# Performance work log

Measured on AMD Instinct MI355X. Metric: run time of the kernel, lower is better.

The kernel has to match this reference:

```python
import jax, jax.numpy as jnp
import numpy as np
import math

B, N, D, K = 8, 2048, 1024, 128
PI = math.pi


def setup_inputs() -> dict:
    key = jax.random.key(0)
    ks = jax.random.split(key, 4)
    x = jax.random.normal(ks[0], (B, N, D), dtype=jnp.float32)
    W_proj = jax.random.normal(ks[1], (D, 6 * K), dtype=jnp.float32) * (D ** -0.5)
    # structured bias init as in OscillatorProjection._init_weights
    b = np.zeros(6 * K, np.float32)
    groups = [K // 4, K // 2, K - K // 4 - K // 2]
    centers = [0.3, 0.65, 0.97]
    off = 3 * K
    for n_k, c in zip(groups, centers):
        b[off:off + n_k] = math.log(c / (1.0 - c))
        off += n_k
    b[4 * K:5 * K] = math.log(0.65 / 0.35)
    b[5 * K:] = -2.0
    b_proj = jnp.asarray(b)
    omega_base = jnp.exp(jnp.linspace(math.log(2.0 * PI / N), math.log(PI * (1.0 - 1.0 / K)), K)).astype(jnp.float32)
    W_phase = jax.random.normal(ks[2], (D, K), dtype=jnp.float32) * 0.001
    b_phase = jnp.zeros((K,), jnp.float32)
    W_res = jax.random.normal(ks[3], (4 * K - 2, D), dtype=jnp.float32) * 0.002
    lambda_pcg = jnp.float32(0.5)
    res_scale = jnp.float32(0.05)
    return dict(x=x, W_proj=W_proj, b_proj=b_proj, omega_base=omega_base,
                W_phase=W_phase, b_phase=b_phase, W_res=W_res,
                lambda_pcg=lambda_pcg, res_scale=res_scale)


def _resonance_scan(alpha, drive):
    # linear recurrence r_t = alpha_t * r_{t-1} + d_t, r_0 = 0, along axis=1
    def combine(e1, e2):
        a1, b1 = e1
        a2, b2 = e2
        return (a2 * a1, a2 * b1 + b2)
    _, r = jax.lax.associative_scan(combine, (alpha, drive), axis=1)
    return r


def reference(x, W_proj, b_proj, omega_base, W_phase, b_phase, W_res, lambda_pcg, res_scale):
    _, n, _ = x.shape
    out = x @ W_proj + b_proj  # [B, n, 6K]
    A_r, Om_r, Ph_r, Ga_r, Go_r, Be_r = jnp.split(out, 6, axis=-1)
    A = jnp.minimum(jax.nn.softplus(A_r), 3.0)
    omega = jnp.clip(jax.nn.sigmoid(Om_r) * PI + omega_base, 1e-4, PI - 1e-4)
    phi = jnp.tanh(Ph_r) * PI
    alpha = jax.nn.sigmoid(Ga_r)
    g_out = jax.nn.sigmoid(Go_r)
    beta = jax.nn.sigmoid(Be_r)
    positions = jnp.log1p(jnp.arange(n, dtype=jnp.float32)).reshape(1, n, 1)
    angle = omega * positions + phi
    cos_a = jnp.cos(angle)
    sin_a = jnp.sin(angle)
    drive = (1.0 - alpha) * A
    # fused real/imag scan sharing alpha (mirrors the fused Triton path)
    r = _resonance_scan(jnp.concatenate([alpha, alpha], axis=-1),
                        jnp.concatenate([drive * cos_a, drive * sin_a], axis=-1))
    r_r, r_i = r[..., :K], r[..., K:]
    readout = r_r * cos_a + r_i * sin_a
    r_r = r_r - beta * readout * cos_a
    r_i = r_i - beta * readout * sin_a
    # state norm: rescale only when |r| > 1
    modulus = jnp.sqrt(r_r ** 2 + r_i ** 2 + 1e-8)
    scale = jnp.maximum(modulus, 1.0)
    r_r = r_r / scale
    r_i = r_i / scale
    # rotate into the oscillator frame
    rho_re = r_r * cos_a + r_i * sin_a
    rho_im = -r_r * sin_a + r_i * cos_a
    rho_norm = jnp.sqrt(rho_re ** 2 + rho_im ** 2 + 1e-6)
    pq = x @ W_phase + b_phase
    align = (rho_re * jnp.cos(pq) + rho_im * jnp.sin(pq)) / rho_norm
    gate = jax.nn.sigmoid(lambda_pcg * align)
    rho_re = gate * rho_re
    rho_im = gate * rho_im
    # SCPM: adjacent-oscillator complex cross products -> 4K-2 features
    cross_re = rho_re[..., :-1] * rho_re[..., 1:] + rho_im[..., :-1] * rho_im[..., 1:]
    cross_im = rho_im[..., :-1] * rho_re[..., 1:] - rho_re[..., :-1] * rho_im[..., 1:]
    feats = jnp.concatenate([g_out * rho_re, g_out * rho_im, cross_re, cross_im], axis=-1)
    return x + res_scale * (feats @ W_res)
```

## Files before the change

kernel.cpp:

```cpp
#include <hip/hip_runtime.h>
#include <math.h>

#define PI_F 3.14159265358979323846f
#define SEG 128
#define SLEN 16
typedef unsigned short u16;
typedef __attribute__((ext_vector_type(8))) short bf16x8;
typedef __attribute__((ext_vector_type(4))) float f32x4;

__device__ __forceinline__ float sigmoidf_(float x){ return __fdividef(1.0f, 1.0f+__expf(-x)); }
__device__ __forceinline__ float softplusf_(float x){
    return fmaxf(x, 0.f) + __logf(1.f + __expf(-fabsf(x)));
}
__device__ __forceinline__ float tanhpi_(float x){
    float t = __expf(-2.f*fabsf(x));
    float th = __fdividef(1.f - t, 1.f + t);
    return copysignf(th, x)*PI_F;
}
__device__ __forceinline__ void fsincos(float a, float* s, float* c){
    float r = a * 0.15915494309189535f;
    r = r - floorf(r);
#if __has_builtin(__builtin_amdgcn_sinf)
    *s = __builtin_amdgcn_sinf(r);
    *c = __builtin_amdgcn_cosf(r);
#else
    float t = r * 6.283185307179586f;
    *s = __sinf(t); *c = __cosf(t);
#endif
}
__device__ __forceinline__ u16 f2bf(float f){
    unsigned u = __float_as_uint(f);
    return (u16)((u + 0x7FFFu + ((u>>16)&1u)) >> 16);
}
__device__ __forceinline__ float b2f(u16 v){
    return __uint_as_float(((unsigned)v)<<16);
}
__device__ __forceinline__ void gl_lds16(const u16* g, u16* l){
    __builtin_amdgcn_global_load_lds((const __attribute__((address_space(1))) void*)g,
                                     (__attribute__((address_space(3))) void*)l, 16, 0, 0);
}

__global__ __launch_bounds__(256) void k_cvt_x(const float* __restrict__ x, u16* __restrict__ xb){
    size_t i = ((size_t)blockIdx.x*256 + threadIdx.x)*8;
    float4 v0 = *(const float4*)&x[i];
    float4 v1 = *(const float4*)&x[i+4];
    ushort4 a = make_ushort4(f2bf(v0.x),f2bf(v0.y),f2bf(v0.z),f2bf(v0.w));
    ushort4 b = make_ushort4(f2bf(v1.x),f2bf(v1.y),f2bf(v1.z),f2bf(v1.w));
    *(ushort4*)&xb[i]   = a;
    *(ushort4*)&xb[i+4] = b;
}

__global__ __launch_bounds__(256) void k_tcvt(const float* __restrict__ W, u16* __restrict__ Wt,
                                              int K, int Ns, int KD){
    __shared__ float s[32][33];
    const int tx = threadIdx.x & 31, ty = threadIdx.x >> 5;
    const int k0 = blockIdx.y*32, n0 = blockIdx.x*32;
    #pragma unroll
    for (int i=0;i<4;i++){
        int k = k0 + ty + i*8;
        s[ty+i*8][tx] = (k < K) ? W[(size_t)k*Ns + n0 + tx] : 0.f;
    }
    __syncthreads();
    #pragma unroll
    for (int i=0;i<4;i++){
        int n = n0 + ty + i*8;
        Wt[(size_t)n*KD + k0 + tx] = f2bf(s[tx][ty+i*8]);
    }
}

__global__ __launch_bounds__(512,1) void k_mm1(
    const u16* __restrict__ A,
    const u16* __restrict__ Bt,
    const float* __restrict__ bp, const float* __restrict__ bph,
    u16* __restrict__ C)
{
    __shared__ u16 sm[3*16384];
    const int bid = blockIdx.x;
    const int swz = (bid & 7)*32 + (bid >> 3);
    const int by = swz >> 2, bx = swz & 3;
    const int r0 = by*256, c0 = bx*256;
    const int tid = threadIdx.x;
    const int w = tid >> 6, lane = tid & 63;
    const int wm = w >> 2, wn = w & 3;
    const int lr = lane & 15, lk = lane >> 4;

    const u16* gA = A  + (size_t)(r0 + w*32 + (lane>>2))*1024 + (lane&3)*8;
    const u16* gB = Bt + (size_t)(c0 + w*32 + (lane>>2))*1024 + (lane&3)*8;
    const int ldsA = w*1024;
    const int ldsB = 8192 + w*1024;

    const int aoff = (wm*128 + lr)*32 + lk*8;
    const int boff = 8192 + (wn*64 + lr)*32 + lk*8;

    f32x4 acc[8][4] = {};

    #pragma unroll
    for (int j=0;j<2;j++){
        gl_lds16(gA + j*16*1024,      sm + ldsA + j*512);
        gl_lds16(gB + j*16*1024,      sm + ldsB + j*512);
    }
    #pragma unroll
    for (int j=0;j<2;j++){
        gl_lds16(gA + j*16*1024 + 32, sm + 16384 + ldsA + j*512);
        gl_lds16(gB + j*16*1024 + 32, sm + 16384 + ldsB + j*512);
    }
    asm volatile("s_waitcnt vmcnt(4)" ::: "memory");
    __builtin_amdgcn_s_barrier();
    __builtin_amdgcn_sched_barrier(0);

    for (int k=0; k<32; ++k){
        const u16* bufp = sm + (k%3)*16384;
        u16*       bufn = sm + ((k+2)%3)*16384;
        const int  k0n  = (k+2)*32;
        bf16x8 af[4], bfr[4];

        #pragma unroll
        for (int m=0;m<4;m++) af[m]  = *(const bf16x8*)&bufp[aoff + m*512];
        #pragma unroll
        for (int n=0;n<4;n++) bfr[n] = *(const bf16x8*)&bufp[boff + n*512];
        if (k < 30){
            gl_lds16(gA + k0n,           bufn + ldsA);
            gl_lds16(gA + 16*1024 + k0n, bufn + ldsA + 512);
        }
        __builtin_amdgcn_s_barrier();
        __builtin_amdgcn_sched_barrier(0);
        asm volatile("s_waitcnt lgkmcnt(0)" ::: "memory");
        __builtin_amdgcn_sched_barrier(0);
        __builtin_amdgcn_s_setprio(1);
        #pragma unroll
        for (int m=0;m<4;m++)
            #pragma unroll
            for (int n=0;n<4;n++)
                acc[m][n] = __builtin_amdgcn_mfma_f32_16x16x32_bf16(af[m], bfr[n], acc[m][n],0,0,0);
        __builtin_amdgcn_s_setprio(0);
        __builtin_amdgcn_s_barrier();
        __builtin_amdgcn_sched_barrier(0);

        #pragma unroll
        for (int m=0;m<4;m++) af[m] = *(const bf16x8*)&bufp[aoff + (m+4)*512];
        if (k < 30){
            gl_lds16(gB + k0n,           bufn + ldsB);
            gl_lds16(gB + 16*1024 + k0n, bufn + ldsB + 512);
        }
        __builtin_amdgcn_s_barrier();
        __builtin_amdgcn_sched_barrier(0);
        asm volatile("s_waitcnt lgkmcnt(0)" ::: "memory");
        __builtin_amdgcn_sched_barrier(0);
        __builtin_amdgcn_s_setprio(1);
        #pragma unroll
        for (int m=0;m<4;m++)
            #pragma unroll
            for (int n=0;n<4;n++)
                acc[m+4][n] = __builtin_amdgcn_mfma_f32_16x16x32_bf16(af[m], bfr[n], acc[m+4][n],0,0,0);
        __builtin_amdgcn_s_setprio(0);
        if (k < 30)       asm volatile("s_waitcnt vmcnt(4)" ::: "memory");
        else if (k == 30) asm volatile("s_waitcnt vmcnt(0)" ::: "memory");
        __builtin_amdgcn_s_barrier();
        __builtin_amdgcn_sched_barrier(0);
    }

    if (c0 + wn*64 < 896){
        #pragma unroll
        for (int n=0;n<4;n++){
            const int col = c0 + wn*64 + n*16 + lr;
            const float bl = (col < 768) ? bp[col] : bph[col-768];
            #pragma unroll
            for (int m=0;m<8;m++){
                const int row = r0 + wm*128 + m*16 + lk*4;
                #pragma unroll
                for (int r=0;r<4;r++)
                    C[(size_t)(row+r)*896 + col] = f2bf(acc[m][n][r] + bl);
            }
        }
    }
}

__global__ __launch_bounds__(256) void k_mm2(
    const u16* __restrict__ A,
    const u16* __restrict__ Bt,
    const u16* __restrict__ Xb,
    const float* __restrict__ rs_p,
    float* __restrict__ O)
{
    const int bid = blockIdx.x;
    const int swz = (bid & 7)*128 + (bid >> 3);
    const int by = swz >> 3, bx = swz & 7;

    __shared__ u16 As[128*32];
    __shared__ u16 Bs[128*32];
    const int tid = threadIdx.x;
    const int w = tid>>6, lane = tid&63;
    const int wm = w>>1, wn = w&1;
    const int r0 = by*128, c0 = bx*128;

    const u16* ga[2]; const u16* gb[2]; u16 *la[2], *lb[2];
    #pragma unroll
    for (int i=0;i<2;i++){
        ga[i] = A  + (size_t)(r0 + w*32 + i*16 + (lane>>2))*512 + (lane&3)*8;
        gb[i] = Bt + (size_t)(c0 + w*32 + i*16 + (lane>>2))*512 + (lane&3)*8;
        la[i] = As + w*1024 + i*512;
        lb[i] = Bs + w*1024 + i*512;
    }
    const int lr = lane&15, lk = lane>>4;
    const int ao = (wm*64 + lr)*32 + lk*8;
    const int bo = (wn*64 + lr)*32 + lk*8;

    f32x4 acc[4][4] = {};
    for (int k0=0; k0<512; k0+=32){
        gl_lds16(ga[0]+k0, la[0]); gl_lds16(ga[1]+k0, la[1]);
        gl_lds16(gb[0]+k0, lb[0]); gl_lds16(gb[1]+k0, lb[1]);
        __syncthreads();
        bf16x8 af[4], bfr[4];
        #pragma unroll
        for (int m=0;m<4;m++) af[m]  = *(const bf16x8*)&As[ao + m*512];
        #pragma unroll
        for (int n=0;n<4;n++) bfr[n] = *(const bf16x8*)&Bs[bo + n*512];
        #pragma unroll
        for (int m=0;m<4;m++)
            #pragma unroll
            for (int n=0;n<4;n++)
                acc[m][n] = __builtin_amdgcn_mfma_f32_16x16x32_bf16(af[m], bfr[n], acc[m][n], 0,0,0);
        __syncthreads();
    }
    const float rs = rs_p[0];
    #pragma unroll
    for (int n=0;n<4;n++){
        int col = c0 + wn*64 + n*16 + lr;
        #pragma unroll
        for (int m=0;m<4;m++){
            int row = r0 + wm*64 + m*16 + lk*4;
            #pragma unroll
            for (int r=0;r<4;r++){
                size_t idx = (size_t)(row+r)*1024 + col;
                O[idx] = b2f(Xb[idx]) + rs*acc[m][n][r];
            }
        }
    }
}

__global__ __launch_bounds__(128) void k_s1(
    const u16* __restrict__ C1,
    const float* __restrict__ omega_base,
    float* __restrict__ Ag, float* __restrict__ Br, float* __restrict__ Bi)
{
    const int k = threadIdx.x;
    const int seg = blockIdx.x, b = blockIdx.y;
    const float ob = omega_base[k];
    const int n0 = seg*SLEN;
    float aag = 1.f, br = 0.f, bi = 0.f;
    #pragma unroll 4
    for (int s=0; s<SLEN; s++){
        const int n = n0 + s;
        const u16* row = C1 + (size_t)(b*2048+n)*896;
        float Ar = b2f(row[k]);
        float Om = b2f(row[128+k]);
        float Ph = b2f(row[256+k]);
        float Ga = b2f(row[384+k]);
        float alpha = sigmoidf_(Ga);
        float A = fminf(softplusf_(Ar), 3.0f);
        float omega = fminf(fmaxf(sigmoidf_(Om)*PI_F + ob, 1e-4f), PI_F-1e-4f);
        float phi = tanhpi_(Ph);
        float pos = __logf(1.f + (float)n);
        float sa, ca; fsincos(fmaf(omega, pos, phi), &sa, &ca);
        float drive = (1.f-alpha)*A;
        aag *= alpha;
        br = fmaf(alpha, br, drive*ca);
        bi = fmaf(alpha, bi, drive*sa);
    }
    const size_t o = (size_t)(b*SEG + seg)*128 + k;
    Ag[o] = aag; Br[o] = br; Bi[o] = bi;
}

__global__ __launch_bounds__(256) void k_s2(
    const float* __restrict__ Ag, const float* __restrict__ Br, const float* __restrict__ Bi,
    float* __restrict__ Pr, float* __restrict__ Pi)
{
    const int gid = blockIdx.x*256 + threadIdx.x;
    const int b = gid >> 7, k = gid & 127;
    float pr = 0.f, pi = 0.f;
    #pragma unroll 8
    for (int seg=0; seg<SEG; seg++){
        const size_t o = (size_t)(b*SEG + seg)*128 + k;
        float a = Ag[o], r = Br[o], i = Bi[o];
        Pr[o] = pr; Pi[o] = pi;
        pr = fmaf(a, pr, r);
        pi = fmaf(a, pi, i);
    }
}

__global__ __launch_bounds__(128) void k_s3(
    const u16* __restrict__ C1,
    const float* __restrict__ omega_base,
    const float* __restrict__ lam_p,
    const float* __restrict__ Pr, const float* __restrict__ Pi,
    u16* __restrict__ F)
{
    const int k = threadIdx.x;
    const int seg = blockIdx.x, b = blockIdx.y;
    const float ob = omega_base[k];
    const float lam = lam_p[0];
    __shared__ float sre[2][129], sim[2][129];

    const size_t po = (size_t)(b*SEG + seg)*128 + k;
    float rr = Pr[po], ri = Pi[po];
    const int n0 = seg*SLEN;

    #pragma unroll 2
    for (int s=0; s<SLEN; s++){
        const int n = n0 + s;
        const u16* row = C1 + (size_t)(b*2048+n)*896;
        float Ar = b2f(row[k]);
        float Om = b2f(row[128+k]);
        float Ph = b2f(row[256+k]);
        float Ga = b2f(row[384+k]);
        float Go = b2f(row[512+k]);
        float Be = b2f(row[640+k]);
        float pq = b2f(row[768+k]);
        float alpha = sigmoidf_(Ga);
        float A = fminf(softplusf_(Ar), 3.0f);
        float omega = fminf(fmaxf(sigmoidf_(Om)*PI_F + ob, 1e-4f), PI_F-1e-4f);
        float phi = tanhpi_(Ph);
        float pos = __logf(1.f + (float)n);
        float sa, ca; fsincos(fmaf(omega, pos, phi), &sa, &ca);
        float drive = (1.f-alpha)*A;
        rr = fmaf(alpha, rr, drive*ca);
        ri = fmaf(alpha, ri, drive*sa);
        float readout = rr*ca + ri*sa;
        float beta = sigmoidf_(Be);
        float r2r = rr - beta*readout*ca;
        float r2i = ri - beta*readout*sa;
        float m2 = r2r*r2r + r2i*r2i + 1e-8f;
        float inv = fminf(rsqrtf(m2), 1.0f);
        r2r *= inv; r2i *= inv;
        float rho_re =  r2r*ca + r2i*sa;
        float rho_im = -r2r*sa + r2i*ca;
        float rho2 = rho_re*rho_re + rho_im*rho_im + 1e-6f;
        float spq, cpq; fsincos(pq, &spq, &cpq);
        float align = (rho_re*cpq + rho_im*spq)*rsqrtf(rho2);
        float gate = sigmoidf_(lam*align);
        rho_re *= gate; rho_im *= gate;
        float go = sigmoidf_(Go);

        const int buf = s & 1;
        sre[buf][k] = rho_re; sim[buf][k] = rho_im;
        __syncthreads();

        u16* frow = F + (size_t)(b*2048+n)*512;
        frow[k]       = f2bf(go*rho_re);
        frow[128 + k] = f2bf(go*rho_im);
        if (k < 127){
            float nre = sre[buf][k+1], nim = sim[buf][k+1];
            frow[256 + k] = f2bf(rho_re*nre + rho_im*nim);
            frow[383 + k] = f2bf(rho_im*nre - rho_re*nim);
        } else {
            frow[510] = 0; frow[511] = 0;
        }
    }
}

extern "C" void kernel_launch(void* const* d_in, const int* in_sizes, int n_in,
                              void* d_out, int out_size, void* d_ws, size_t ws_size,
                              hipStream_t stream)
{
    const float* x   = (const float*)d_in[0];
    const float* Wp  = (const float*)d_in[1];
    const float* bp  = (const float*)d_in[2];
    const float* ob  = (const float*)d_in[3];
    const float* Wph = (const float*)d_in[4];
    const float* bph = (const float*)d_in[5];
    const float* Wr  = (const float*)d_in[6];
    const float* lam = (const float*)d_in[7];
    const float* rs  = (const float*)d_in[8];
    float* out = (float*)d_out;

    char* ws = (char*)d_ws;
    u16*   C1  = (u16*)  (ws + 0);
    float* Ag  = (float*)(ws + 29360128);
    float* Brr = (float*)(ws + 29884416);
    float* Bii = (float*)(ws + 30408704);
    float* Pr  = (float*)(ws + 30932992);
    float* Pi  = (float*)(ws + 31457280);
    u16*   F   = (u16*)  (ws + 31981568);
    u16*   Wt  = (u16*)  (ws + 48758784);
    u16*   Wrt = (u16*)  (ws + 50855936);
    u16*   Xb  = (u16*)  (ws + 58720256);

    dim3 blk(256);
    hipMemsetAsync(Wt, 0, 2097152, stream);
    hipLaunchKernelGGL(k_cvt_x, dim3(8192),   blk, 0, stream, x, Xb);
    hipLaunchKernelGGL(k_tcvt,  dim3(24,32),  blk, 0, stream, Wp,  Wt,            1024, 768,  1024);
    hipLaunchKernelGGL(k_tcvt,  dim3(4,32),   blk, 0, stream, Wph, Wt + 768*1024, 1024, 128,  1024);
    hipLaunchKernelGGL(k_tcvt,  dim3(32,16),  blk, 0, stream, Wr,  Wrt,           510,  1024, 512);
    hipLaunchKernelGGL(k_mm1,   dim3(256),    dim3(512), 0, stream, Xb, Wt, bp, bph, C1);
    hipLaunchKernelGGL(k_s1,    dim3(SEG,8),  dim3(128), 0, stream, C1, ob, Ag, Brr, Bii);
    hipLaunchKernelGGL(k_s2,    dim3(4),      blk, 0, stream, Ag, Brr, Bii, Pr, Pi);
    hipLaunchKernelGGL(k_s3,    dim3(SEG,8),  dim3(128), 0, stream, C1, ob, lam, Pr, Pi, F);
    hipLaunchKernelGGL(k_mm2,   dim3(1024),   blk, 0, stream, F, Wrt, Xb, rs, out);
}
```

Before: 143.8 us.

## Swizzle LDS layout in mm1 and port mm2 to triple-buffered 256x256 pipeline

Applies an XOR swizzle to the global-to-LDS load column and the matching fragment read offsets in k_mm1, to reduce LDS bank conflicts. Rewrites k_mm2 to use the same 512-thread, 256x256-tile, triple-buffered pipeline as k_mm1, with split A/B prefetch, barriers and setprio around the MFMA blocks, and launches 256 blocks instead of 1024. This is meant to raise data reuse and overlap global loads with MFMA work in the output GEMM. The cost is fewer blocks (256 over the GPU's CUs), which lowers occupancy and parallelism, and more complex synchronisation.

```diff
diff --git a/kernel.cpp b/kernel.cpp
--- a/kernel.cpp
+++ b/kernel.cpp
@@ -68,6 +68,7 @@
     }
 }
 
+
 __global__ __launch_bounds__(512,1) void k_mm1(
     const u16* __restrict__ A,
     const u16* __restrict__ Bt,
@@ -84,13 +85,15 @@
     const int wm = w >> 2, wn = w & 3;
     const int lr = lane & 15, lk = lane >> 4;
 
-    const u16* gA = A  + (size_t)(r0 + w*32 + (lane>>2))*1024 + (lane&3)*8;
-    const u16* gB = Bt + (size_t)(c0 + w*32 + (lane>>2))*1024 + (lane&3)*8;
+    const int cg = ((lane&3) ^ ((lane>>3)&3))*8;
+    const u16* gA = A  + (size_t)(r0 + w*32 + (lane>>2))*1024 + cg;
+    const u16* gB = Bt + (size_t)(c0 + w*32 + (lane>>2))*1024 + cg;
     const int ldsA = w*1024;
     const int ldsB = 8192 + w*1024;
 
-    const int aoff = (wm*128 + lr)*32 + lk*8;
-    const int boff = 8192 + (wn*64 + lr)*32 + lk*8;
+    const int cs = (lk ^ ((lr>>1)&3))*8;
+    const int aoff = (wm*128 + lr)*32 + cs;
+    const int boff = 8192 + (wn*64 + lr)*32 + cs;
 
     f32x4 acc[8][4] = {};
 
@@ -175,60 +178,107 @@
     }
 }
 
-__global__ __launch_bounds__(256) void k_mm2(
+__global__ __launch_bounds__(512,1) void k_mm2(
     const u16* __restrict__ A,
     const u16* __restrict__ Bt,
     const u16* __restrict__ Xb,
     const float* __restrict__ rs_p,
     float* __restrict__ O)
 {
+    __shared__ u16 sm[3*16384];
     const int bid = blockIdx.x;
-    const int swz = (bid & 7)*128 + (bid >> 3);
-    const int by = swz >> 3, bx = swz & 7;
-
-    __shared__ u16 As[128*32];
-    __shared__ u16 Bs[128*32];
+    const int swz = (bid & 7)*32 + (bid >> 3);
+    const int by = swz >> 2, bx = swz & 3;
+    const int r0 = by*256, c0 = bx*256;
     const int tid = threadIdx.x;
-    const int w = tid>>6, lane = tid&63;
-    const int wm = w>>1, wn = w&1;
-    const int r0 = by*128, c0 = bx*128;
-
-    const u16* ga[2]; const u16* gb[2]; u16 *la[2], *lb[2];
-    #pragma unroll
-    for (int i=0;i<2;i++){
-        ga[i] = A  + (size_t)(r0 + w*32 + i*16 + (lane>>2))*512 + (lane&3)*8;
-        gb[i] = Bt + (size_t)(c0 + w*32 + i*16 + (lane>>2))*512 + (lane&3)*8;
-        la[i] = As + w*1024 + i*512;
-        lb[i] = Bs + w*1024 + i*512;
-    }
-    const int lr = lane&15, lk = lane>>4;
-    const int ao = (wm*64 + lr)*32 + lk*8;
-    const int bo = (wn*64 + lr)*32 + lk*8;
-
-    f32x4 acc[4][4] = {};
-    for (int k0=0; k0<512; k0+=32){
-        gl_lds16(ga[0]+k0, la[0]); gl_lds16(ga[1]+k0, la[1]);
-        gl_lds16(gb[0]+k0, lb[0]); gl_lds16(gb[1]+k0, lb[1]);
-        __syncthreads();
+    const int w = tid >> 6, lane = tid & 63;
+    const int wm = w >> 2, wn = w & 3;
+    const int lr = lane & 15, lk = lane >> 4;
+
+    const int cg = ((lane&3) ^ ((lane>>3)&3))*8;
+    const u16* gA = A  + (size_t)(r0 + w*32 + (lane>>2))*512 + cg;
+    const u16* gB = Bt + (size_t)(c0 + w*32 + (lane>>2))*512 + cg;
+    const int ldsA = w*1024;
+    const int ldsB = 8192 + w*1024;
+
+    const int cs = (lk ^ ((lr>>1)&3))*8;
+    const int aoff = (wm*128 + lr)*32 + cs;
+    const int boff = 8192 + (wn*64 + lr)*32 + cs;
+
+    f32x4 acc[8][4] = {};
+
+    #pragma unroll
+    for (int j=0;j<2;j++){
+        gl_lds16(gA + j*16*512,      sm + ldsA + j*512);
+        gl_lds16(gB + j*16*512,      sm + ldsB + j*512);
+    }
+    #pragma unroll
+    for (int j=0;j<2;j++){
+        gl_lds16(gA + j*16*512 + 32, sm + 16384 + ldsA + j*512);
+        gl_lds16(gB + j*16*512 + 32, sm + 16384 + ldsB + j*512);
+    }
+    asm volatile("s_waitcnt vmcnt(4)" ::: "memory");
+    __builtin_amdgcn_s_barrier();
+    __builtin_amdgcn_sched_barrier(0);
+
+    for (int k=0; k<16; ++k){
+        const u16* bufp = sm + (k%3)*16384;
+        u16*       bufn = sm + ((k+2)%3)*16384;
+        const int  k0n  = (k+2)*32;
         bf16x8 af[4], bfr[4];
-        #pragma unroll
-        for (int m=0;m<4;m++) af[m]  = *(const bf16x8*)&As[ao + m*512];
-        #pragma unroll
-        for (int n=0;n<4;n++) bfr[n] = *(const bf16x8*)&Bs[bo + n*512];
+
+        #pragma unroll
+        for (int m=0;m<4;m++) af[m]  = *(const bf16x8*)&bufp[aoff + m*512];
+        #pragma unroll
+        for (int n=0;n<4;n++) bfr[n] = *(const bf16x8*)&bufp[boff + n*512];
+        if (k < 14){
+            gl_lds16(gA + k0n,          bufn + ldsA);
+            gl_lds16(gA + 16*512 + k0n, bufn + ldsA + 512);
+        }
+        __builtin_amdgcn_s_barrier();
+        __builtin_amdgcn_sched_barrier(0);
+        asm volatile("s_waitcnt lgkmcnt(0)" ::: "memory");
+        __builtin_amdgcn_sched_barrier(0);
+        __builtin_amdgcn_s_setprio(1);
         #pragma unroll
         for (int m=0;m<4;m++)
             #pragma unroll
             for (int n=0;n<4;n++)
-                acc[m][n] = __builtin_amdgcn_mfma_f32_16x16x32_bf16(af[m], bfr[n], acc[m][n], 0,0,0);
-        __syncthreads();
-    }
+                acc[m][n] = __builtin_amdgcn_mfma_f32_16x16x32_bf16(af[m], bfr[n], acc[m][n],0,0,0);
+        __builtin_amdgcn_s_setprio(0);
+        __builtin_amdgcn_s_barrier();
+        __builtin_amdgcn_sched_barrier(0);
+
+        #pragma unroll
+        for (int m=0;m<4;m++) af[m] = *(const bf16x8*)&bufp[aoff + (m+4)*512];
+        if (k < 14){
+            gl_lds16(gB + k0n,          bufn + ldsB);
+            gl_lds16(gB + 16*512 + k0n, bufn + ldsB + 512);
+        }
+        __builtin_amdgcn_s_barrier();
+        __builtin_amdgcn_sched_barrier(0);
+        asm volatile("s_waitcnt lgkmcnt(0)" ::: "memory");
+        __builtin_amdgcn_sched_barrier(0);
+        __builtin_amdgcn_s_setprio(1);
+        #pragma unroll
+        for (int m=0;m<4;m++)
+            #pragma unroll
+            for (int n=0;n<4;n++)
+                acc[m+4][n] = __builtin_amdgcn_mfma_f32_16x16x32_bf16(af[m], bfr[n], acc[m+4][n],0,0,0);
+        __builtin_amdgcn_s_setprio(0);
+        if (k < 14)       asm volatile("s_waitcnt vmcnt(4)" ::: "memory");
+        else if (k == 14) asm volatile("s_waitcnt vmcnt(0)" ::: "memory");
+        __builtin_amdgcn_s_barrier();
+        __builtin_amdgcn_sched_barrier(0);
+    }
+
     const float rs = rs_p[0];
     #pragma unroll
     for (int n=0;n<4;n++){
-        int col = c0 + wn*64 + n*16 + lr;
-        #pragma unroll
-        for (int m=0;m<4;m++){
-            int row = r0 + wm*64 + m*16 + lk*4;
+        const int col = c0 + wn*64 + n*16 + lr;
+        #pragma unroll
+        for (int m=0;m<8;m++){
+            const int row = r0 + wm*128 + m*16 + lk*4;
             #pragma unroll
             for (int r=0;r<4;r++){
                 size_t idx = (size_t)(row+r)*1024 + col;
@@ -395,5 +445,5 @@
     hipLaunchKernelGGL(k_s1,    dim3(SEG,8),  dim3(128), 0, stream, C1, ob, Ag, Brr, Bii);
     hipLaunchKernelGGL(k_s2,    dim3(4),      blk, 0, stream, Ag, Brr, Bii, Pr, Pi);
     hipLaunchKernelGGL(k_s3,    dim3(SEG,8),  dim3(128), 0, stream, C1, ob, lam, Pr, Pi, F);
-    hipLaunchKernelGGL(k_mm2,   dim3(1024),   blk, 0, stream, F, Wrt, Xb, rs, out);
-}
+    hipLaunchKernelGGL(k_mm2,   dim3(256),    dim3(512), 0, stream, F, Wrt, Xb, rs, out);
+}
```

Measured after the change: 166.4 us. 15.7% more time.
